# Optimization experiments

Hardware: AMD Instinct MI355X
Metric: run time of the kernel (lower is better)

Reference implementation:

```python
import jax, jax.numpy as jnp
import numpy as np

GAMMA = 1.0

def setup_inputs() -> dict:
    key = jax.random.key(0)
    kx, ky = jax.random.split(key)
    x = jax.random.normal(kx, (8192, 256), dtype=jnp.float32)
    y = jax.random.normal(ky, (8192, 256), dtype=jnp.float32)
    return {"x": x, "y": y}

def reference(x, y):
    # Pairwise squared distance via norms + GEMM:
    # ||x_i - y_j||^2 = ||x_i||^2 - 2 x_i . y_j + ||y_j||^2
    x_sq = jnp.sum(x * x, axis=-1)  # [N]
    y_sq = jnp.sum(y * y, axis=-1)  # [M]
    cross = jnp.einsum('nd,md->nm', x, y)  # [N, M]
    sq_dist = x_sq[:, None] - 2.0 * cross + y_sq[None, :]
    return jnp.exp(-GAMMA * sq_dist)
```

## Files before the change

kernel.cpp:

```cpp
#include <hip/hip_runtime.h>
#include <hip/hip_bf16.h>

#define NROWS 8192
#define DDIM  256
#define BM 128
#define BN 128
#define BK 64

typedef __attribute__((ext_vector_type(4))) float f32x4;
typedef __attribute__((ext_vector_type(8))) short bf16x8;
typedef __attribute__((ext_vector_type(4))) short short4v;

__device__ inline short f2bf(float f) {
    union { float f; unsigned u; } c; c.f = f;
    unsigned u = c.u;
    u += 0x7fffu + ((u >> 16) & 1u);
    return (short)(u >> 16);
}

__global__ __launch_bounds__(256) void convert_norms_kernel(
    const float* __restrict__ x, const float* __restrict__ y,
    short* __restrict__ xb, short* __restrict__ yb,
    float* __restrict__ xsq, float* __restrict__ ysq) {
    int row  = blockIdx.x * 4 + (threadIdx.x >> 6);
    int lane = threadIdx.x & 63;
    const float* src; short* dstb; float* dstn; int r;
    if (row < NROWS) { r = row;        src = x + (size_t)r * DDIM; dstb = xb + (size_t)r * DDIM; dstn = xsq; }
    else             { r = row - NROWS; src = y + (size_t)r * DDIM; dstb = yb + (size_t)r * DDIM; dstn = ysq; }
    f32x4 v = __builtin_nontemporal_load(&((const f32x4*)src)[lane]);
    short4v o;
    #pragma unroll
    for (int j = 0; j < 4; ++j) o[j] = f2bf(v[j]);
    ((short4v*)dstb)[lane] = o;
    float s = v[0]*v[0] + v[1]*v[1] + v[2]*v[2] + v[3]*v[3];
    #pragma unroll
    for (int off = 32; off > 0; off >>= 1) s += __shfl_xor(s, off, 64);
    if (lane == 0) dstn[r] = s;
}

__global__ __launch_bounds__(256) void rbf_gemm_bf16_kernel(
    const char* __restrict__ Xb, const char* __restrict__ Yb,
    const float* __restrict__ xsq, const float* __restrict__ ysq,
    float* __restrict__ out) {
    __shared__ char lds[2 * BM * BK * 2];
    char* As = lds;
    char* Bs = lds + BM * BK * 2;

    const int tid  = threadIdx.x;
    const int lane = tid & 63;
    const int wid  = tid >> 6;

    const int bid = blockIdx.x;
    const int xcd = bid & 7;
    const int c   = bid >> 3;
    const int by  = (xcd >> 2) * 32 + (c >> 4);
    const int bx  = (xcd & 3)  * 16 + (c & 15);
    const int brow = by * BM;
    const int bcol = bx * BN;
    const int wr = (wid >> 1) * 64;
    const int wc = (wid & 1) * 64;

    const char* aS[4]; const char* bS[4];
    #pragma unroll
    for (int i = 0; i < 4; ++i) {
        const int q    = i * 4096 + tid * 16;
        const int row  = q >> 7;
        const int colb = q & 127;
        const int sc   = colb ^ ((row & 7) << 4);
        aS[i] = Xb + (size_t)(brow + row) * 512 + sc;
        bS[i] = Yb + (size_t)(bcol + row) * 512 + sc;
    }

    f32x4 acc[4][4] = {};

    for (int ks = 0; ks < DDIM / BK; ++ks) {
        #pragma unroll
        for (int i = 0; i < 4; ++i) {
            __builtin_amdgcn_global_load_lds(
                (const __attribute__((address_space(1))) void*)(aS[i] + ks * 128),
                (__attribute__((address_space(3))) void*)(As + i * 4096 + wid * 1024),
                16, 0, 0);
            __builtin_amdgcn_global_load_lds(
                (const __attribute__((address_space(1))) void*)(bS[i] + ks * 128),
                (__attribute__((address_space(3))) void*)(Bs + i * 4096 + wid * 1024),
                16, 0, 0);
        }
        __syncthreads();

        #pragma unroll
        for (int kk = 0; kk < 2; ++kk) {
            const int kb = kk * 64 + ((lane >> 4) << 4);
            bf16x8 af[4], bf[4];
            #pragma unroll
            for (int m = 0; m < 4; ++m) {
                const int r = wr + m * 16 + (lane & 15);
                af[m] = *(const bf16x8*)(As + r * 128 + (kb ^ ((r & 7) << 4)));
            }
            #pragma unroll
            for (int n = 0; n < 4; ++n) {
                const int cc = wc + n * 16 + (lane & 15);
                bf[n] = *(const bf16x8*)(Bs + cc * 128 + (kb ^ ((cc & 7) << 4)));
            }
            #pragma unroll
            for (int m = 0; m < 4; ++m)
                #pragma unroll
                for (int n = 0; n < 4; ++n)
                    acc[m][n] = __builtin_amdgcn_mfma_f32_16x16x32_bf16(
                        af[m], bf[n], acc[m][n], 0, 0, 0);
        }
        __syncthreads();
    }

    const int r0 = brow + wr + ((lane >> 4) << 2);
    const int c0 = bcol + wc + (lane & 15);
    float xs[4][4];
    #pragma unroll
    for (int m = 0; m < 4; ++m)
        #pragma unroll
        for (int j = 0; j < 4; ++j)
            xs[m][j] = xsq[r0 + m * 16 + j];
    #pragma unroll
    for (int n = 0; n < 4; ++n) {
        const float ys = ysq[c0 + n * 16];
        #pragma unroll
        for (int m = 0; m < 4; ++m) {
            #pragma unroll
            for (int j = 0; j < 4; ++j) {
                const int row = r0 + m * 16 + j;
                const float v = __expf(2.0f * acc[m][n][j] - xs[m][j] - ys);
                out[(size_t)row * NROWS + c0 + n * 16] = v;
            }
        }
    }
}

__global__ __launch_bounds__(256) void row_norms_kernel(
    const float* __restrict__ x, const float* __restrict__ y,
    float* __restrict__ sq) {
    int row  = blockIdx.x * 4 + (threadIdx.x >> 6);
    int lane = threadIdx.x & 63;
    const float* src = (row < NROWS) ? (x + (size_t)row * DDIM)
                                     : (y + (size_t)(row - NROWS) * DDIM);
    f32x4 v = ((const f32x4*)src)[lane];
    float s = v[0]*v[0] + v[1]*v[1] + v[2]*v[2] + v[3]*v[3];
    #pragma unroll
    for (int off = 32; off > 0; off >>= 1) s += __shfl_xor(s, off, 64);
    if (lane == 0) sq[row] = s;
}

__global__ __launch_bounds__(256) void rbf_gemm_f32_kernel(
    const float* __restrict__ X, const float* __restrict__ Y,
    const float* __restrict__ xsq, const float* __restrict__ ysq,
    float* __restrict__ out) {
    __shared__ char lds[2 * BM * BK * 2];
    char* As = lds;
    char* Bs = lds + BM * BK * 2;
    const int tid  = threadIdx.x;
    const int lane = tid & 63;
    const int wid  = tid >> 6;
    const int brow = blockIdx.y * BM;
    const int bcol = blockIdx.x * BN;
    const int wr = (wid >> 1) * 64;
    const int wc = (wid & 1) * 64;
    const int srow  = tid >> 1;
    const int shalf = tid & 1;
    const float* aptr = X + (size_t)(brow + srow) * DDIM + shalf * 32;
    const float* bptr = Y + (size_t)(bcol + srow) * DDIM + shalf * 32;
    const int swz = (srow & 7) << 4;
    f32x4 acc[4][4] = {};
    for (int ks = 0; ks < DDIM / BK; ++ks) {
        __syncthreads();
        #pragma unroll
        for (int i = 0; i < 4; ++i) {
            f32x4 a0 = ((const f32x4*)(aptr + ks * BK))[2*i];
            f32x4 a1 = ((const f32x4*)(aptr + ks * BK))[2*i + 1];
            f32x4 b0 = ((const f32x4*)(bptr + ks * BK))[2*i];
            f32x4 b1 = ((const f32x4*)(bptr + ks * BK))[2*i + 1];
            bf16x8 av, bv;
            #pragma unroll
            for (int j = 0; j < 4; ++j) {
                av[j]   = f2bf(a0[j]);  av[4+j] = f2bf(a1[j]);
                bv[j]   = f2bf(b0[j]);  bv[4+j] = f2bf(b1[j]);
            }
            const int cb = shalf * 64 + i * 16;
            *(bf16x8*)(As + srow * 128 + (cb ^ swz)) = av;
            *(bf16x8*)(Bs + srow * 128 + (cb ^ swz)) = bv;
        }
        __syncthreads();
        #pragma unroll
        for (int kk = 0; kk < 2; ++kk) {
            const int kb = kk * 64 + ((lane >> 4) << 4);
            bf16x8 af[4], bf[4];
            #pragma unroll
            for (int m = 0; m < 4; ++m) {
                const int r = wr + m * 16 + (lane & 15);
                af[m] = *(const bf16x8*)(As + r * 128 + (kb ^ ((r & 7) << 4)));
            }
            #pragma unroll
            for (int n = 0; n < 4; ++n) {
                const int cc = wc + n * 16 + (lane & 15);
                bf[n] = *(const bf16x8*)(Bs + cc * 128 + (kb ^ ((cc & 7) << 4)));
            }
            #pragma unroll
            for (int m = 0; m < 4; ++m)
                #pragma unroll
                for (int n = 0; n < 4; ++n)
                    acc[m][n] = __builtin_amdgcn_mfma_f32_16x16x32_bf16(
                        af[m], bf[n], acc[m][n], 0, 0, 0);
        }
    }
    const int r0 = brow + wr + ((lane >> 4) << 2);
    const int c0 = bcol + wc + (lane & 15);
    float xs[4][4];
    #pragma unroll
    for (int m = 0; m < 4; ++m)
        #pragma unroll
        for (int j = 0; j < 4; ++j)
            xs[m][j] = xsq[r0 + m * 16 + j];
    #pragma unroll
    for (int n = 0; n < 4; ++n) {
        const float ys = ysq[c0 + n * 16];
        #pragma unroll
        for (int m = 0; m < 4; ++m) {
            #pragma unroll
            for (int j = 0; j < 4; ++j) {
                const int row = r0 + m * 16 + j;
                const float v = __expf(2.0f * acc[m][n][j] - xs[m][j] - ys);
                out[(size_t)row * NROWS + c0 + n * 16] = v;
            }
        }
    }
}

extern "C" void kernel_launch(void* const* d_in, const int* in_sizes, int n_in,
                              void* d_out, int out_size, void* d_ws, size_t ws_size,
                              hipStream_t stream) {
    const float* x = (const float*)d_in[0];
    const float* y = (const float*)d_in[1];
    float* out = (float*)d_out;

    const size_t xb_bytes = (size_t)NROWS * DDIM * 2;
    const size_t needed   = 2 * xb_bytes + 2 * NROWS * 4;

    if (ws_size >= needed) {
        char*  ws  = (char*)d_ws;
        short* xb  = (short*)ws;
        short* yb  = (short*)(ws + xb_bytes);
        float* xsq = (float*)(ws + 2 * xb_bytes);
        float* ysq = xsq + NROWS;
        convert_norms_kernel<<<dim3(2 * NROWS / 4), dim3(256), 0, stream>>>(
            x, y, xb, yb, xsq, ysq);
        rbf_gemm_bf16_kernel<<<dim3(4096), dim3(256), 0, stream>>>(
            (const char*)xb, (const char*)yb, xsq, ysq, out);
    } else {
        float* sq = (float*)d_ws;
        row_norms_kernel<<<dim3(2 * NROWS / 4), dim3(256), 0, stream>>>(x, y, sq);
        rbf_gemm_f32_kernel<<<dim3(NROWS / BN, NROWS / BM), dim3(256), 0, stream>>>(
            x, y, sq, sq + NROWS, out);
    }
}
```

Before: 67.04 us.

## Halve K-tile, merge A/B LDS buffer, transpose MFMA for vectorized epilogue stores

The bf16 GEMM kernel now uses BK=32 with a single 16KB LDS buffer that holds A and B interleaved per line. This halves LDS usage and adds a launch bound of 4 blocks per SM to raise occupancy. MFMA operands are swapped so each lane holds 4 consecutive output columns, which enables f32x4 loads of ysq and 16-byte vectorized output stores instead of scalar stores. In exchange the kernel runs twice as many K-iterations and barriers, with less MFMA work between syncs.

```diff
diff --git a/kernel.cpp b/kernel.cpp
--- a/kernel.cpp
+++ b/kernel.cpp
@@ -5,7 +5,7 @@
 #define DDIM  256
 #define BM 128
 #define BN 128
-#define BK 64
+#define BK 32
 
 typedef __attribute__((ext_vector_type(4))) float f32x4;
 typedef __attribute__((ext_vector_type(8))) short bf16x8;
@@ -38,13 +38,11 @@
     if (lane == 0) dstn[r] = s;
 }
 
-__global__ __launch_bounds__(256) void rbf_gemm_bf16_kernel(
+__global__ __launch_bounds__(256, 4) void rbf_gemm_bf16_kernel(
     const char* __restrict__ Xb, const char* __restrict__ Yb,
     const float* __restrict__ xsq, const float* __restrict__ ysq,
     float* __restrict__ out) {
-    __shared__ char lds[2 * BM * BK * 2];
-    char* As = lds;
-    char* Bs = lds + BM * BK * 2;
+    __shared__ char lds[BM * 128];
 
     const int tid  = threadIdx.x;
     const int lane = tid & 63;
@@ -60,76 +58,64 @@
     const int wr = (wid >> 1) * 64;
     const int wc = (wid & 1) * 64;
 
-    const char* aS[4]; const char* bS[4];
+    const char* src[4];
     #pragma unroll
     for (int i = 0; i < 4; ++i) {
         const int q    = i * 4096 + tid * 16;
-        const int row  = q >> 7;
-        const int colb = q & 127;
-        const int sc   = colb ^ ((row & 7) << 4);
-        aS[i] = Xb + (size_t)(brow + row) * 512 + sc;
-        bS[i] = Yb + (size_t)(bcol + row) * 512 + sc;
-    }
+        const int line = q >> 7;
+        const int scol = (q & 127) ^ ((line & 7) << 4);
+        src[i] = (scol < 64)
+            ? Xb + (size_t)(brow + line) * 512 + scol
+            : Yb + (size_t)(bcol + line) * 512 + (scol - 64);
+    }
+
+    const int swz = (lane & 7) << 4;
+    const int kq  = (lane >> 4) << 4;
 
     f32x4 acc[4][4] = {};
 
     for (int ks = 0; ks < DDIM / BK; ++ks) {
         #pragma unroll
-        for (int i = 0; i < 4; ++i) {
+        for (int i = 0; i < 4; ++i)
             __builtin_amdgcn_global_load_lds(
-                (const __attribute__((address_space(1))) void*)(aS[i] + ks * 128),
-                (__attribute__((address_space(3))) void*)(As + i * 4096 + wid * 1024),
+                (const __attribute__((address_space(1))) void*)(src[i] + ks * 64),
+                (__attribute__((address_space(3))) void*)(lds + i * 4096 + wid * 1024),
                 16, 0, 0);
-            __builtin_amdgcn_global_load_lds(
-                (const __attribute__((address_space(1))) void*)(bS[i] + ks * 128),
-                (__attribute__((address_space(3))) void*)(Bs + i * 4096 + wid * 1024),
-                16, 0, 0);
-        }
-        __syncthreads();
-
-        #pragma unroll
-        for (int kk = 0; kk < 2; ++kk) {
-            const int kb = kk * 64 + ((lane >> 4) << 4);
-            bf16x8 af[4], bf[4];
-            #pragma unroll
-            for (int m = 0; m < 4; ++m) {
-                const int r = wr + m * 16 + (lane & 15);
-                af[m] = *(const bf16x8*)(As + r * 128 + (kb ^ ((r & 7) << 4)));
-            }
-            #pragma unroll
-            for (int n = 0; n < 4; ++n) {
-                const int cc = wc + n * 16 + (lane & 15);
-                bf[n] = *(const bf16x8*)(Bs + cc * 128 + (kb ^ ((cc & 7) << 4)));
-            }
-            #pragma unroll
-            for (int m = 0; m < 4; ++m)
-                #pragma unroll
-                for (int n = 0; n < 4; ++n)
-                    acc[m][n] = __builtin_amdgcn_mfma_f32_16x16x32_bf16(
-                        af[m], bf[n], acc[m][n], 0, 0, 0);
-        }
-        __syncthreads();
-    }
-
-    const int r0 = brow + wr + ((lane >> 4) << 2);
-    const int c0 = bcol + wc + (lane & 15);
-    float xs[4][4];
-    #pragma unroll
-    for (int m = 0; m < 4; ++m)
-        #pragma unroll
-        for (int j = 0; j < 4; ++j)
-            xs[m][j] = xsq[r0 + m * 16 + j];
-    #pragma unroll
-    for (int n = 0; n < 4; ++n) {
-        const float ys = ysq[c0 + n * 16];
+        __syncthreads();
+
+        bf16x8 af[4], bf[4];
         #pragma unroll
         for (int m = 0; m < 4; ++m) {
-            #pragma unroll
-            for (int j = 0; j < 4; ++j) {
-                const int row = r0 + m * 16 + j;
-                const float v = __expf(2.0f * acc[m][n][j] - xs[m][j] - ys);
-                out[(size_t)row * NROWS + c0 + n * 16] = v;
-            }
+            const int r = wr + m * 16 + (lane & 15);
+            af[m] = *(const bf16x8*)(lds + r * 128 + (kq ^ swz));
+        }
+        #pragma unroll
+        for (int n = 0; n < 4; ++n) {
+            const int r = wc + n * 16 + (lane & 15);
+            bf[n] = *(const bf16x8*)(lds + r * 128 + ((64 + kq) ^ swz));
+        }
+        #pragma unroll
+        for (int m = 0; m < 4; ++m)
+            #pragma unroll
+            for (int n = 0; n < 4; ++n)
+                acc[m][n] = __builtin_amdgcn_mfma_f32_16x16x32_bf16(
+                    bf[n], af[m], acc[m][n], 0, 0, 0);
+        __syncthreads();
+    }
+
+    #pragma unroll
+    for (int m = 0; m < 4; ++m) {
+        const int R  = brow + wr + m * 16 + (lane & 15);
+        const float xsv = xsq[R];
+        #pragma unroll
+        for (int n = 0; n < 4; ++n) {
+            const int C = bcol + wc + n * 16 + ((lane >> 4) << 2);
+            const f32x4 ysv = *(const f32x4*)&ysq[C];
+            f32x4 v;
+            #pragma unroll
+            for (int j = 0; j < 4; ++j)
+                v[j] = __expf(2.0f * acc[m][n][j] - xsv - ysv[j]);
+            *(f32x4*)&out[(size_t)R * NROWS + C] = v;
         }
     }
 }
@@ -152,9 +138,9 @@
     const float* __restrict__ X, const float* __restrict__ Y,
     const float* __restrict__ xsq, const float* __restrict__ ysq,
     float* __restrict__ out) {
-    __shared__ char lds[2 * BM * BK * 2];
+    __shared__ char lds[2 * BM * 64 * 2 * 2];
     char* As = lds;
-    char* Bs = lds + BM * BK * 2;
+    char* Bs = lds + BM * 64 * 2;
     const int tid  = threadIdx.x;
     const int lane = tid & 63;
     const int wid  = tid >> 6;
@@ -168,14 +154,14 @@
     const float* bptr = Y + (size_t)(bcol + srow) * DDIM + shalf * 32;
     const int swz = (srow & 7) << 4;
     f32x4 acc[4][4] = {};
-    for (int ks = 0; ks < DDIM / BK; ++ks) {
+    for (int ks = 0; ks < DDIM / 64; ++ks) {
         __syncthreads();
         #pragma unroll
         for (int i = 0; i < 4; ++i) {
-            f32x4 a0 = ((const f32x4*)(aptr + ks * BK))[2*i];
-            f32x4 a1 = ((const f32x4*)(aptr + ks * BK))[2*i + 1];
-            f32x4 b0 = ((const f32x4*)(bptr + ks * BK))[2*i];
-            f32x4 b1 = ((const f32x4*)(bptr + ks * BK))[2*i + 1];
+            f32x4 a0 = ((const f32x4*)(aptr + ks * 64))[2*i];
+            f32x4 a1 = ((const f32x4*)(aptr + ks * 64))[2*i + 1];
+            f32x4 b0 = ((const f32x4*)(bptr + ks * 64))[2*i];
+            f32x4 b1 = ((const f32x4*)(bptr + ks * 64))[2*i + 1];
             bf16x8 av, bv;
             #pragma unroll
             for (int j = 0; j < 4; ++j) {
```

Result: slower. 100.2 us (+49.5%).

## Stage RBF output tile through LDS for coalesced vectorized global stores

Applied to the files above, without the earlier changes.

Swaps the MFMA operand order so each lane's accumulator holds four consecutive columns, then writes the exp results through a swizzled LDS staging buffer and stores full 512-byte rows to global memory with float4 writes. The old epilogue issued scalar strided stores, which is costly because the 256 MB output write dominates the kernel. The staging adds barriers and extra LDS traffic in the epilogue. It also replaces BK with a literal 64 and remaps which rows each wave handles.

```diff
diff --git a/kernel.cpp b/kernel.cpp
--- a/kernel.cpp
+++ b/kernel.cpp
@@ -106,31 +106,40 @@
                 #pragma unroll
                 for (int n = 0; n < 4; ++n)
                     acc[m][n] = __builtin_amdgcn_mfma_f32_16x16x32_bf16(
-                        af[m], bf[n], acc[m][n], 0, 0, 0);
-        }
-        __syncthreads();
-    }
-
-    const int r0 = brow + wr + ((lane >> 4) << 2);
-    const int c0 = bcol + wc + (lane & 15);
-    float xs[4][4];
-    #pragma unroll
-    for (int m = 0; m < 4; ++m)
-        #pragma unroll
-        for (int j = 0; j < 4; ++j)
-            xs[m][j] = xsq[r0 + m * 16 + j];
-    #pragma unroll
-    for (int n = 0; n < 4; ++n) {
-        const float ys = ysq[c0 + n * 16];
-        #pragma unroll
-        for (int m = 0; m < 4; ++m) {
-            #pragma unroll
-            for (int j = 0; j < 4; ++j) {
-                const int row = r0 + m * 16 + j;
-                const float v = __expf(2.0f * acc[m][n][j] - xs[m][j] - ys);
-                out[(size_t)row * NROWS + c0 + n * 16] = v;
-            }
-        }
+                        bf[n], af[m], acc[m][n], 0, 0, 0);
+        }
+        __syncthreads();
+    }
+
+    const int rl  = ((wid >> 1) << 4) + (lane & 15);
+    const int rgl = rl + ((rl & 16) ? 48 : 0);
+    f32x4 ys4[4];
+    #pragma unroll
+    for (int n = 0; n < 4; ++n)
+        ys4[n] = *(const f32x4*)&ysq[bcol + wc + n * 16 + ((lane >> 4) << 2)];
+
+    #pragma unroll
+    for (int m = 0; m < 4; ++m) {
+        const float xsv = xsq[brow + m * 16 + rgl];
+        #pragma unroll
+        for (int n = 0; n < 4; ++n) {
+            f32x4 v;
+            #pragma unroll
+            for (int j = 0; j < 4; ++j)
+                v[j] = __expf(2.0f * acc[m][n][j] - xsv - ys4[n][j]);
+            const int slot = ((wid & 1) << 4) + (n << 2) + (lane >> 4);
+            *(f32x4*)(lds + rl * 512 + ((slot ^ (rl & 7)) << 4)) = v;
+        }
+        __syncthreads();
+        #pragma unroll
+        for (int p = 0; p < 4; ++p) {
+            const int rr    = (p << 3) + (tid >> 5);
+            const int slot2 = tid & 31;
+            const f32x4 v = *(const f32x4*)(lds + rr * 512 + ((slot2 ^ (rr & 7)) << 4));
+            const int growr = brow + (m << 4) + rr + ((rr & 16) ? 48 : 0);
+            *(f32x4*)&out[(size_t)growr * NROWS + bcol + (slot2 << 2)] = v;
+        }
+        __syncthreads();
     }
 }
 
@@ -152,9 +161,9 @@
     const float* __restrict__ X, const float* __restrict__ Y,
     const float* __restrict__ xsq, const float* __restrict__ ysq,
     float* __restrict__ out) {
-    __shared__ char lds[2 * BM * BK * 2];
+    __shared__ char lds[2 * BM * 64 * 2];
     char* As = lds;
-    char* Bs = lds + BM * BK * 2;
+    char* Bs = lds + BM * 64 * 2;
     const int tid  = threadIdx.x;
     const int lane = tid & 63;
     const int wid  = tid >> 6;
@@ -168,14 +177,14 @@
     const float* bptr = Y + (size_t)(bcol + srow) * DDIM + shalf * 32;
     const int swz = (srow & 7) << 4;
     f32x4 acc[4][4] = {};
-    for (int ks = 0; ks < DDIM / BK; ++ks) {
+    for (int ks = 0; ks < DDIM / 64; ++ks) {
         __syncthreads();
         #pragma unroll
         for (int i = 0; i < 4; ++i) {
-            f32x4 a0 = ((const f32x4*)(aptr + ks * BK))[2*i];
-            f32x4 a1 = ((const f32x4*)(aptr + ks * BK))[2*i + 1];
-            f32x4 b0 = ((const f32x4*)(bptr + ks * BK))[2*i];
-            f32x4 b1 = ((const f32x4*)(bptr + ks * BK))[2*i + 1];
+            f32x4 a0 = ((const f32x4*)(aptr + ks * 64))[2*i];
+            f32x4 a1 = ((const f32x4*)(aptr + ks * 64))[2*i + 1];
+            f32x4 b0 = ((const f32x4*)(bptr + ks * 64))[2*i];
+            f32x4 b1 = ((const f32x4*)(bptr + ks * 64))[2*i + 1];
             bf16x8 av, bv;
             #pragma unroll
             for (int j = 0; j < 4; ++j) {
```

New measurement: 70.25 us. 4.8% more time.
